# Optimization experiments

Measured on AMD Instinct MI355X. Metric: run time of the kernel, lower is better.

The kernel has to match this reference:

```python
import jax, jax.numpy as jnp
import numpy as np
from jax import lax

B, N, C_IN = 8, 4096, 64
NPOINT, NSAMPLE, RADIUS = 1024, 32, 0.2
BN_EPS = 1e-3  # keras BatchNormalization default epsilon


def _fps(pts):
    """Farthest point sampling on a single cloud pts: (N, 3) -> (NPOINT,) int32."""
    n = pts.shape[0]
    def step(carry, _):
        dist, far = carry
        c = pts[far]                                  # (3,)
        d = jnp.sum((pts - c) ** 2, axis=-1)          # (N,)
        dist = jnp.minimum(dist, d)
        nxt = jnp.argmax(dist).astype(jnp.int32)
        return (dist, nxt), far
    init = (jnp.full((n,), 1e10, pts.dtype), jnp.array(0, jnp.int32))
    _, idx = lax.scan(step, init, None, length=NPOINT)
    return idx


def _ball_query(xyz, new_xyz):
    """xyz: (B,N,3), new_xyz: (B,P,3) -> idx (B,P,NSAMPLE) int32.
    First NSAMPLE point indices within RADIUS of each centroid (in original
    order); slots beyond the in-ball count are filled with the first in-ball
    index, matching the PointNet++ CUDA query_ball_point semantics."""
    n = xyz.shape[1]
    # squared distances via the expansion trick to avoid a (B,P,N,3) temp
    d2 = (jnp.sum(new_xyz ** 2, -1)[:, :, None]
          + jnp.sum(xyz ** 2, -1)[:, None, :]
          - 2.0 * jnp.einsum('bpc,bnc->bpn', new_xyz, xyz))  # (B,P,N)
    in_ball = d2 < RADIUS ** 2
    cand = jnp.where(in_ball, jnp.arange(n, dtype=jnp.int32)[None, None, :], n)
    neg_top, _ = lax.top_k(-cand, NSAMPLE)   # NSAMPLE smallest indices
    idx = -neg_top                           # ascending order
    first = idx[..., :1]                     # centroid itself is always in-ball
    idx = jnp.where(idx == n, first, idx)
    return idx


def _group(feats, idx):
    """feats: (B,N,C), idx: (B,P,S) -> (B,P,S,C) gather per batch."""
    return jax.vmap(lambda f, i: f[i])(feats, idx)


def _mlp_layer(x, W, g, b, m, v):
    # 1x1 conv (no bias) + BN (inference stats) + ReLU
    x = jnp.einsum('bpsc,cd->bpsd', x, W)
    x = (x - m) * lax.rsqrt(v + BN_EPS) * g + b
    return jax.nn.relu(x)


def setup_inputs() -> dict:
    key = jax.random.key(0)
    ks = jax.random.split(key, 8)
    xyz = jax.random.uniform(ks[0], (B, N, 3), dtype=jnp.float32)
    points = jax.random.normal(ks[1], (B, N, C_IN), dtype=jnp.float32)
    c0 = 3 + C_IN  # use_xyz=True
    W0 = jax.random.normal(ks[2], (c0, 64), jnp.float32) / np.sqrt(c0)
    W1 = jax.random.normal(ks[3], (64, 64), jnp.float32) / np.sqrt(64.0)
    W2 = jax.random.normal(ks[4], (64, 128), jnp.float32) / np.sqrt(64.0)
    def bn(c):
        return (jnp.ones((c,), jnp.float32), jnp.zeros((c,), jnp.float32),
                jnp.zeros((c,), jnp.float32), jnp.ones((c,), jnp.float32))
    g0, b0, m0, v0 = bn(64)
    g1, b1, m1, v1 = bn(64)
    g2, b2, m2, v2 = bn(128)
    return dict(xyz=xyz, points=points,
                W0=W0, g0=g0, b0=b0, m0=m0, v0=v0,
                W1=W1, g1=g1, b1=b1, m1=m1, v1=v1,
                W2=W2, g2=g2, b2=b2, m2=m2, v2=v2)


def reference(xyz, points,
              W0, g0, b0, m0, v0,
              W1, g1, b1, m1, v1,
              W2, g2, b2, m2, v2):
    # --- sample_and_group ---
    fps_idx = jax.vmap(_fps)(xyz)                            # (B,P)
    new_xyz = jnp.take_along_axis(xyz, fps_idx[:, :, None], axis=1)  # (B,P,3)
    idx = _ball_query(xyz, new_xyz)                          # (B,P,S)
    grouped_xyz = _group(xyz, idx) - new_xyz[:, :, None, :]  # (B,P,S,3)
    grouped_pts = _group(points, idx)                        # (B,P,S,C)
    new_points = jnp.concatenate([grouped_xyz, grouped_pts], axis=-1)
    # --- shared per-point MLP (1x1 conv + BN + ReLU) ---
    new_points = _mlp_layer(new_points, W0, g0, b0, m0, v0)
    new_points = _mlp_layer(new_points, W1, g1, b1, m1, v1)
    new_points = _mlp_layer(new_points, W2, g2, b2, m2, v2)
    # --- max pool over the neighborhood axis ---
    new_points = jnp.max(new_points, axis=2)                 # (B,P,128)
    return new_xyz, new_points, idx
```

## Files before the change

### kernel.cpp

```cpp
#include <hip/hip_runtime.h>
#include <stdint.h>

#define BN_EPS 0.001f

typedef float v2f __attribute__((ext_vector_type(2)));


struct FpsSh {
  float px[4096], py[4096], pz[4096];
  unsigned long long wk[2][4];
  int curh[32];
};

struct WrkSh {
  float W0s[67 * 64];
  float W1s[64 * 64];
  float sh[64 * 36];
  float h0T[64 * 34];
  float s0c[64], t0c[64], s1c[64], t1c[64], s2c[128], t2c[128];
  float idxs[4 * 32];
  float cent[4 * 3];
};

union AllSh {
  FpsSh f;
  WrkSh w;
};

__global__ __launch_bounds__(256) void fused_kernel(
    const float* __restrict__ xyz, const float* __restrict__ points,
    const float* __restrict__ W0, const float* __restrict__ g0,
    const float* __restrict__ b0, const float* __restrict__ m0,
    const float* __restrict__ v0, const float* __restrict__ W1,
    const float* __restrict__ g1, const float* __restrict__ b1,
    const float* __restrict__ m1, const float* __restrict__ v1,
    const float* __restrict__ W2, const float* __restrict__ g2,
    const float* __restrict__ b2, const float* __restrict__ m2,
    const float* __restrict__ v2, float* __restrict__ new_xyz,
    float* __restrict__ new_points, float* __restrict__ idxf,
    unsigned int* __restrict__ prog) {
  __shared__ __align__(16) AllSh smem;
  const int bid = blockIdx.x;
  const int t = threadIdx.x;

  if (bid < 8) {
#pragma clang fp contract(off)
    float* px = smem.f.px;
    float* py = smem.f.py;
    float* pz = smem.f.pz;
    int* curh = smem.f.curh;
    auto& wk = smem.f.wk;
    const int lane = t & 63, wid = t >> 6;
    const int b = bid;
    const float* X = xyz + (size_t)b * 4096 * 3;
    float* out = new_xyz + (size_t)b * 1024 * 3;
    v2f x[8], y[8], z[8], dist[8];
#pragma unroll
    for (int j = 0; j < 8; ++j) {
      const int n0 = (2 * j) * 256 + t;
      const int n1 = (2 * j + 1) * 256 + t;
      x[j].x = X[n0 * 3 + 0]; x[j].y = X[n1 * 3 + 0];
      y[j].x = X[n0 * 3 + 1]; y[j].y = X[n1 * 3 + 1];
      z[j].x = X[n0 * 3 + 2]; z[j].y = X[n1 * 3 + 2];
      px[n0] = x[j].x; py[n0] = y[j].x; pz[n0] = z[j].x;
      px[n1] = x[j].y; py[n1] = y[j].y; pz[n1] = z[j].y;
      dist[j] = (v2f){1e10f, 1e10f};
    }
    __syncthreads();
    int cur = 0;
    for (int cc = 0; cc < 32; ++cc) {
      for (int ii = 0; ii < 32; ++ii) {
        const int it = cc * 32 + ii;
        if (t == 0) curh[ii] = cur;
        const float cx = px[cur], cy = py[cur], cz = pz[cur];
        const v2f cxv = {cx, cx}, cyv = {cy, cy}, czv = {cz, cz};
        float bestv = -1.0f;
        int bestj = 0;
#pragma unroll
        for (int j = 0; j < 8; ++j) {
          v2f dx = x[j] - cxv, dy = y[j] - cyv, dz = z[j] - czv;
          v2f d = dx * dx + dy * dy;
          d = d + dz * dz;
          v2f nd = __builtin_elementwise_min(dist[j], d);
          dist[j] = nd;
          if (nd.x > bestv) { bestv = nd.x; bestj = 2 * j; }
          if (nd.y > bestv) { bestv = nd.y; bestj = 2 * j + 1; }
        }
        const int besti = bestj * 256 + t;
        unsigned long long key =
            ((unsigned long long)__float_as_uint(bestv) << 32) | (unsigned)(~besti);
#define DPP_STEP(CTRL)                                                                     \
        {                                                                                  \
          unsigned lo_ = (unsigned)key, hi_ = (unsigned)(key >> 32);                       \
          unsigned ls = (unsigned)__builtin_amdgcn_update_dpp((int)lo_, (int)lo_, CTRL, 0xf, 0xf, false); \
          unsigned hs = (unsigned)__builtin_amdgcn_update_dpp((int)hi_, (int)hi_, CTRL, 0xf, 0xf, false); \
          unsigned long long sk = ((unsigned long long)hs << 32) | ls;                     \
          if (sk > key) key = sk;                                                          \
        }
        DPP_STEP(0x111)
        DPP_STEP(0x112)
        DPP_STEP(0x114)
        DPP_STEP(0x118)
        DPP_STEP(0x142)
        DPP_STEP(0x143)
#undef DPP_STEP
        const unsigned whi = (unsigned)__builtin_amdgcn_readlane((int)(key >> 32), 63);
        const unsigned wlo = (unsigned)__builtin_amdgcn_readlane((int)key, 63);
        if (lane == 0) wk[it & 1][wid] = ((unsigned long long)whi << 32) | wlo;
        __syncthreads();
        const unsigned long long k0 = wk[it & 1][0], k1 = wk[it & 1][1];
        const unsigned long long k2 = wk[it & 1][2], k3 = wk[it & 1][3];
        unsigned long long b01 = (k1 > k0) ? k1 : k0;
        unsigned long long b23 = (k3 > k2) ? k3 : k2;
        unsigned long long bk = (b23 > b01) ? b23 : b01;
        cur = (int)(~(unsigned)(bk & 0xffffffffull));
      }
      if (t < 32) {
        const int c = curh[t];
        const int p = cc * 32 + t;
        out[p * 3 + 0] = px[c];
        out[p * 3 + 1] = py[c];
        out[p * 3 + 2] = pz[c];
      }
      __syncthreads();
      if (t == 0)
        __hip_atomic_store(&prog[b * 32], (unsigned)(cc * 32 + 32),
                           __ATOMIC_RELEASE, __HIP_MEMORY_SCOPE_AGENT);
    }
    return;
  }

  float* W0s = smem.w.W0s;
  float* W1s = smem.w.W1s;
  float* s0c = smem.w.s0c; float* t0c = smem.w.t0c;
  float* s1c = smem.w.s1c; float* t1c = smem.w.t1c;
  float* s2c = smem.w.s2c; float* t2c = smem.w.t2c;
  for (int i = t; i < 67 * 64; i += 256) W0s[i] = W0[i];
  for (int i = t; i < 64 * 64; i += 256) W1s[i] = W1[i];
  if (t < 64) {
    float s = g0[t] * rsqrtf(v0[t] + BN_EPS); s0c[t] = s; t0c[t] = b0[t] - m0[t] * s;
    float u = g1[t] * rsqrtf(v1[t] + BN_EPS); s1c[t] = u; t1c[t] = b1[t] - m1[t] * u;
  }
  if (t < 128) {
    float s = g2[t] * rsqrtf(v2[t] + BN_EPS); s2c[t] = s; t2c[t] = b2[t] - m2[t] * s;
  }
  __syncthreads();
  const int sgrp = t & 15, dgrp = t >> 4;
  const int dg2 = t & 31, sg2 = t >> 5;
  float* inT = smem.w.sh;
  float* h1T = smem.w.sh;
  float* h0T = smem.w.h0T;
  float* pmax = h0T;

  int kbeg, kend, kstep;
  if (bid >= 256) { kbeg = 2032 + (bid - 256); kend = 2048; kstep = 8; }
  else            { kbeg = bid - 8;            kend = 2032; kstep = 248; }

  for (int k = kbeg; k < kend; k += kstep) {
    const int j = k >> 3, b = k & 7;
    const int pgbase = b * 1024 + j * 4;
    const unsigned need = (unsigned)(j * 4 + 4);
    {
      int guard = 0;
      while (__hip_atomic_load(&prog[b * 32], __ATOMIC_RELAXED,
                               __HIP_MEMORY_SCOPE_AGENT) < need) {
        __builtin_amdgcn_s_sleep(32);
        if (++guard > (1 << 20)) break;
      }
      (void)__hip_atomic_load(&prog[b * 32], __ATOMIC_ACQUIRE,
                              __HIP_MEMORY_SCOPE_AGENT);
    }
    {
#pragma clang fp contract(off)
      const int wv = t >> 6, lane = t & 63;
      const int pg = pgbase + wv;
      const float* X = xyz + (size_t)b * 4096 * 3;
      const float cx = new_xyz[pg * 3 + 0];
      const float cy = new_xyz[pg * 3 + 1];
      const float cz = new_xyz[pg * 3 + 2];
      const float csq = (cx * cx + cy * cy) + cz * cz;
      float* outg = idxf + (size_t)pg * 32;
      float* ol = smem.w.idxs + wv * 32;
      int total = 0;
      int first = -1;
      for (int chunk = 0; chunk < 64; ++chunk) {
        const int n = chunk * 64 + lane;
        const float xx = X[n * 3 + 0], yy = X[n * 3 + 1], zz = X[n * 3 + 2];
        const float sq = (xx * xx + yy * yy) + zz * zz;
        const float dot = fmaf(cz, zz, fmaf(cy, yy, cx * xx));
        const float d2 = (csq + sq) - 2.0f * dot;
        const bool in = d2 < 0.04f;
        const unsigned long long mask = __ballot(in);
        if (first < 0 && mask != 0ull) first = chunk * 64 + __builtin_ctzll(mask);
        if (in) {
          const int pos = total + __builtin_popcountll(mask & ((1ull << lane) - 1ull));
          if (pos < 32) { outg[pos] = (float)n; ol[pos] = (float)n; }
        }
        total += __builtin_popcountll(mask);
        if (total >= 32) break;
      }
      if (total < 32 && first >= 0) {
        const int slot = total + lane;
        if (slot < 32) { outg[slot] = (float)first; ol[slot] = (float)first; }
      }
      if (lane == 0) {
        smem.w.cent[wv * 3 + 0] = cx;
        smem.w.cent[wv * 3 + 1] = cy;
        smem.w.cent[wv * 3 + 2] = cz;
      }
    }
    __syncthreads();
    for (int pp = 0; pp < 4; ++pp) {
      const int pg = pgbase + pp;
      const float cx = smem.w.cent[pp * 3 + 0];
      const float cy = smem.w.cent[pp * 3 + 1];
      const float cz = smem.w.cent[pp * 3 + 2];
      {
        const int s = t >> 3, cg = t & 7;
        const int i = (int)smem.w.idxs[pp * 32 + s];
        const float* Pr = points + ((size_t)b * 4096 + i) * 64 + cg * 8;
        const float4 a = *(const float4*)Pr;
        const float4 c4 = *(const float4*)(Pr + 4);
        const int r = 3 + cg * 8;
        inT[(r + 0) * 34 + s] = a.x;  inT[(r + 1) * 34 + s] = a.y;
        inT[(r + 2) * 34 + s] = a.z;  inT[(r + 3) * 34 + s] = a.w;
        inT[(r + 4) * 34 + s] = c4.x; inT[(r + 5) * 34 + s] = c4.y;
        inT[(r + 6) * 34 + s] = c4.z; inT[(r + 7) * 34 + s] = c4.w;
        if (t < 32) {
          const int i2 = (int)smem.w.idxs[pp * 32 + t];
          const float* Xr = xyz + ((size_t)b * 4096 + i2) * 3;
          inT[0 * 34 + t] = Xr[0] - cx;
          inT[1 * 34 + t] = Xr[1] - cy;
          inT[2 * 34 + t] = Xr[2] - cz;
        }
      }
      __syncthreads();
      {
        float acc[2][4] = {{0, 0, 0, 0}, {0, 0, 0, 0}};
#pragma unroll 4
        for (int c = 0; c < 67; ++c) {
          const float2 a = *(const float2*)&inT[c * 34 + 2 * sgrp];
          const float4 w = *(const float4*)&W0s[c * 64 + 4 * dgrp];
          acc[0][0] = fmaf(a.x, w.x, acc[0][0]); acc[0][1] = fmaf(a.x, w.y, acc[0][1]);
          acc[0][2] = fmaf(a.x, w.z, acc[0][2]); acc[0][3] = fmaf(a.x, w.w, acc[0][3]);
          acc[1][0] = fmaf(a.y, w.x, acc[1][0]); acc[1][1] = fmaf(a.y, w.y, acc[1][1]);
          acc[1][2] = fmaf(a.y, w.z, acc[1][2]); acc[1][3] = fmaf(a.y, w.w, acc[1][3]);
        }
#pragma unroll
        for (int dj = 0; dj < 4; ++dj) {
          const int d = 4 * dgrp + dj;
          const float s = s0c[d], bb = t0c[d];
#pragma unroll
          for (int si = 0; si < 2; ++si) {
            float yv = fmaf(acc[si][dj], s, bb);
            h0T[d * 34 + 2 * sgrp + si] = fmaxf(yv, 0.0f);
          }
        }
      }
      __syncthreads();
      {
        float acc[2][4] = {{0, 0, 0, 0}, {0, 0, 0, 0}};
#pragma unroll 4
        for (int c = 0; c < 64; ++c) {
          const float2 a = *(const float2*)&h0T[c * 34 + 2 * sgrp];
          const float4 w = *(const float4*)&W1s[c * 64 + 4 * dgrp];
          acc[0][0] = fmaf(a.x, w.x, acc[0][0]); acc[0][1] = fmaf(a.x, w.y, acc[0][1]);
          acc[0][2] = fmaf(a.x, w.z, acc[0][2]); acc[0][3] = fmaf(a.x, w.w, acc[0][3]);
          acc[1][0] = fmaf(a.y, w.x, acc[1][0]); acc[1][1] = fmaf(a.y, w.y, acc[1][1]);
          acc[1][2] = fmaf(a.y, w.z, acc[1][2]); acc[1][3] = fmaf(a.y, w.w, acc[1][3]);
        }
#pragma unroll
        for (int dj = 0; dj < 4; ++dj) {
          const int d = 4 * dgrp + dj;
          const float s = s1c[d], bb = t1c[d];
#pragma unroll
          for (int si = 0; si < 2; ++si) {
            float yv = fmaf(acc[si][dj], s, bb);
            h1T[d * 36 + 2 * sgrp + si] = fmaxf(yv, 0.0f);
          }
        }
      }
      __syncthreads();
      {
        float acc[4][4] = {{0,0,0,0},{0,0,0,0},{0,0,0,0},{0,0,0,0}};
#pragma unroll 8
        for (int c = 0; c < 64; ++c) {
          const float4 a = *(const float4*)&h1T[c * 36 + 4 * sg2];
          const float4 w = *(const float4*)(W2 + c * 128 + 4 * dg2);
          acc[0][0] = fmaf(a.x, w.x, acc[0][0]); acc[0][1] = fmaf(a.x, w.y, acc[0][1]);
          acc[0][2] = fmaf(a.x, w.z, acc[0][2]); acc[0][3] = fmaf(a.x, w.w, acc[0][3]);
          acc[1][0] = fmaf(a.y, w.x, acc[1][0]); acc[1][1] = fmaf(a.y, w.y, acc[1][1]);
          acc[1][2] = fmaf(a.y, w.z, acc[1][2]); acc[1][3] = fmaf(a.y, w.w, acc[1][3]);
          acc[2][0] = fmaf(a.z, w.x, acc[2][0]); acc[2][1] = fmaf(a.z, w.y, acc[2][1]);
          acc[2][2] = fmaf(a.z, w.z, acc[2][2]); acc[2][3] = fmaf(a.z, w.w, acc[2][3]);
          acc[3][0] = fmaf(a.w, w.x, acc[3][0]); acc[3][1] = fmaf(a.w, w.y, acc[3][1]);
          acc[3][2] = fmaf(a.w, w.z, acc[3][2]); acc[3][3] = fmaf(a.w, w.w, acc[3][3]);
        }
#pragma unroll
        for (int dj = 0; dj < 4; ++dj) {
          const int d = 4 * dg2 + dj;
          const float s = s2c[d], bb = t2c[d];
          float mx = 0.0f;
#pragma unroll
          for (int si = 0; si < 4; ++si) {
            float yv = fmaf(acc[si][dj], s, bb);
            mx = fmaxf(mx, fmaxf(yv, 0.0f));
          }
          pmax[sg2 * 128 + d] = mx;
        }
      }
      __syncthreads();
      if (t < 128) {
        float mx = pmax[t];
#pragma unroll
        for (int g = 1; g < 8; ++g) mx = fmaxf(mx, pmax[g * 128 + t]);
        new_points[(size_t)pg * 128 + t] = mx;
      }
      __syncthreads();
    }
  }
}

extern "C" void kernel_launch(void* const* d_in, const int* in_sizes, int n_in,
                              void* d_out, int out_size, void* d_ws, size_t ws_size,
                              hipStream_t stream) {
  (void)in_sizes; (void)n_in; (void)out_size; (void)ws_size;
  const float* xyz    = (const float*)d_in[0];
  const float* points = (const float*)d_in[1];
  const float* W0 = (const float*)d_in[2];
  const float* g0 = (const float*)d_in[3];
  const float* b0 = (const float*)d_in[4];
  const float* m0 = (const float*)d_in[5];
  const float* v0 = (const float*)d_in[6];
  const float* W1 = (const float*)d_in[7];
  const float* g1 = (const float*)d_in[8];
  const float* b1 = (const float*)d_in[9];
  const float* m1 = (const float*)d_in[10];
  const float* v1 = (const float*)d_in[11];
  const float* W2 = (const float*)d_in[12];
  const float* g2 = (const float*)d_in[13];
  const float* b2 = (const float*)d_in[14];
  const float* m2 = (const float*)d_in[15];
  const float* v2 = (const float*)d_in[16];

  float* new_xyz    = (float*)d_out;
  float* new_points = new_xyz + 8 * 1024 * 3;
  float* idxf       = new_points + 8 * 1024 * 128;

  unsigned int* prog = (unsigned int*)d_ws;
  hipMemsetAsync(d_ws, 0, 8 * 32 * sizeof(unsigned int), stream);
  fused_kernel<<<264, 256, 0, stream>>>(xyz, points, W0, g0, b0, m0, v0,
                                        W1, g1, b1, m1, v1,
                                        W2, g2, b2, m2, v2,
                                        new_xyz, new_points, idxf, prog);
}
```

Measured before the change: 780.4 us.

## Split tail centroid groups across extra blocks and relax FPS progress signalling

The final 32 centroids per batch were previously handled as groups of four by 8 tail blocks, serialising the work after FPS finishes. The launch grows to 320 blocks so 64 tail blocks each handle one centroid, shortening the critical tail after the last FPS chunk. The progress flag publication changes from a release store to relaxed atomic stores plus an explicit s_waitcnt, and the consumer drops its acquire load in favour of relaxed atomic reads of new_xyz. The aim is to cut fence cost, but this relies on hardware ordering rather than the memory model, and the extra blocks need co-residency to avoid spin deadlock.

```diff
diff --git a/kernel.cpp b/kernel.cpp
--- a/kernel.cpp
+++ b/kernel.cpp
@@ -118,14 +118,19 @@
       if (t < 32) {
         const int c = curh[t];
         const int p = cc * 32 + t;
-        out[p * 3 + 0] = px[c];
-        out[p * 3 + 1] = py[c];
-        out[p * 3 + 2] = pz[c];
-      }
-      __syncthreads();
-      if (t == 0)
+        __hip_atomic_store(&out[p * 3 + 0], px[c], __ATOMIC_RELAXED,
+                           __HIP_MEMORY_SCOPE_AGENT);
+        __hip_atomic_store(&out[p * 3 + 1], py[c], __ATOMIC_RELAXED,
+                           __HIP_MEMORY_SCOPE_AGENT);
+        __hip_atomic_store(&out[p * 3 + 2], pz[c], __ATOMIC_RELAXED,
+                           __HIP_MEMORY_SCOPE_AGENT);
+      }
+      __syncthreads();
+      if (t == 0) {
+        asm volatile("s_waitcnt vmcnt(0)" ::: "memory");
         __hip_atomic_store(&prog[b * 32], (unsigned)(cc * 32 + 32),
-                           __ATOMIC_RELEASE, __HIP_MEMORY_SCOPE_AGENT);
+                           __ATOMIC_RELAXED, __HIP_MEMORY_SCOPE_AGENT);
+      }
     }
     return;
   }
@@ -152,66 +157,63 @@
   float* h0T = smem.w.h0T;
   float* pmax = h0T;
 
-  int kbeg, kend, kstep;
-  if (bid >= 256) { kbeg = 2032 + (bid - 256); kend = 2048; kstep = 8; }
-  else            { kbeg = bid - 8;            kend = 2032; kstep = 248; }
-
-  for (int k = kbeg; k < kend; k += kstep) {
-    const int j = k >> 3, b = k & 7;
-    const int pgbase = b * 1024 + j * 4;
-    const unsigned need = (unsigned)(j * 4 + 4);
-    {
-      int guard = 0;
-      while (__hip_atomic_load(&prog[b * 32], __ATOMIC_RELAXED,
-                               __HIP_MEMORY_SCOPE_AGENT) < need) {
-        __builtin_amdgcn_s_sleep(32);
-        if (++guard > (1 << 20)) break;
-      }
-      (void)__hip_atomic_load(&prog[b * 32], __ATOMIC_ACQUIRE,
-                              __HIP_MEMORY_SCOPE_AGENT);
-    }
+  auto wait_prog = [&](int b, unsigned need) {
+    int guard = 0;
+    while (__hip_atomic_load(&prog[b * 32], __ATOMIC_RELAXED,
+                             __HIP_MEMORY_SCOPE_AGENT) < need) {
+      __builtin_amdgcn_s_sleep(32);
+      if (++guard > (1 << 20)) break;
+    }
+  };
+
+  auto process_group = [&](int b, int p0, int nc) {
     {
 #pragma clang fp contract(off)
       const int wv = t >> 6, lane = t & 63;
-      const int pg = pgbase + wv;
-      const float* X = xyz + (size_t)b * 4096 * 3;
-      const float cx = new_xyz[pg * 3 + 0];
-      const float cy = new_xyz[pg * 3 + 1];
-      const float cz = new_xyz[pg * 3 + 2];
-      const float csq = (cx * cx + cy * cy) + cz * cz;
-      float* outg = idxf + (size_t)pg * 32;
-      float* ol = smem.w.idxs + wv * 32;
-      int total = 0;
-      int first = -1;
-      for (int chunk = 0; chunk < 64; ++chunk) {
-        const int n = chunk * 64 + lane;
-        const float xx = X[n * 3 + 0], yy = X[n * 3 + 1], zz = X[n * 3 + 2];
-        const float sq = (xx * xx + yy * yy) + zz * zz;
-        const float dot = fmaf(cz, zz, fmaf(cy, yy, cx * xx));
-        const float d2 = (csq + sq) - 2.0f * dot;
-        const bool in = d2 < 0.04f;
-        const unsigned long long mask = __ballot(in);
-        if (first < 0 && mask != 0ull) first = chunk * 64 + __builtin_ctzll(mask);
-        if (in) {
-          const int pos = total + __builtin_popcountll(mask & ((1ull << lane) - 1ull));
-          if (pos < 32) { outg[pos] = (float)n; ol[pos] = (float)n; }
-        }
-        total += __builtin_popcountll(mask);
-        if (total >= 32) break;
-      }
-      if (total < 32 && first >= 0) {
-        const int slot = total + lane;
-        if (slot < 32) { outg[slot] = (float)first; ol[slot] = (float)first; }
-      }
-      if (lane == 0) {
-        smem.w.cent[wv * 3 + 0] = cx;
-        smem.w.cent[wv * 3 + 1] = cy;
-        smem.w.cent[wv * 3 + 2] = cz;
+      if (wv < nc) {
+        const int pg = b * 1024 + p0 + wv;
+        const float* X = xyz + (size_t)b * 4096 * 3;
+        const float cx = __hip_atomic_load(&new_xyz[pg * 3 + 0], __ATOMIC_RELAXED,
+                                           __HIP_MEMORY_SCOPE_AGENT);
+        const float cy = __hip_atomic_load(&new_xyz[pg * 3 + 1], __ATOMIC_RELAXED,
+                                           __HIP_MEMORY_SCOPE_AGENT);
+        const float cz = __hip_atomic_load(&new_xyz[pg * 3 + 2], __ATOMIC_RELAXED,
+                                           __HIP_MEMORY_SCOPE_AGENT);
+        const float csq = (cx * cx + cy * cy) + cz * cz;
+        float* outg = idxf + (size_t)pg * 32;
+        float* ol = smem.w.idxs + wv * 32;
+        int total = 0;
+        int first = -1;
+        for (int chunk = 0; chunk < 64; ++chunk) {
+          const int n = chunk * 64 + lane;
+          const float xx = X[n * 3 + 0], yy = X[n * 3 + 1], zz = X[n * 3 + 2];
+          const float sq = (xx * xx + yy * yy) + zz * zz;
+          const float dot = fmaf(cz, zz, fmaf(cy, yy, cx * xx));
+          const float d2 = (csq + sq) - 2.0f * dot;
+          const bool in = d2 < 0.04f;
+          const unsigned long long mask = __ballot(in);
+          if (first < 0 && mask != 0ull) first = chunk * 64 + __builtin_ctzll(mask);
+          if (in) {
+            const int pos = total + __builtin_popcountll(mask & ((1ull << lane) - 1ull));
+            if (pos < 32) { outg[pos] = (float)n; ol[pos] = (float)n; }
+          }
+          total += __builtin_popcountll(mask);
+          if (total >= 32) break;
+        }
+        if (total < 32 && first >= 0) {
+          const int slot = total + lane;
+          if (slot < 32) { outg[slot] = (float)first; ol[slot] = (float)first; }
+        }
+        if (lane == 0) {
+          smem.w.cent[wv * 3 + 0] = cx;
+          smem.w.cent[wv * 3 + 1] = cy;
+          smem.w.cent[wv * 3 + 2] = cz;
+        }
       }
     }
     __syncthreads();
-    for (int pp = 0; pp < 4; ++pp) {
-      const int pg = pgbase + pp;
+    for (int pp = 0; pp < nc; ++pp) {
+      const int pg = b * 1024 + p0 + pp;
       const float cx = smem.w.cent[pp * 3 + 0];
       const float cy = smem.w.cent[pp * 3 + 1];
       const float cz = smem.w.cent[pp * 3 + 2];
@@ -317,6 +319,20 @@
         new_points[(size_t)pg * 128 + t] = mx;
       }
       __syncthreads();
+    }
+  };
+
+  if (bid >= 256) {
+    const int sid = bid - 256;
+    const int b = sid & 7;
+    const int p0 = 1016 + (sid >> 3);
+    wait_prog(b, (unsigned)(p0 + 1));
+    process_group(b, p0, 1);
+  } else {
+    for (int k = bid - 8; k < 2032; k += 248) {
+      const int j = k >> 3, b = k & 7;
+      wait_prog(b, (unsigned)(j * 4 + 4));
+      process_group(b, j * 4, 4);
     }
   }
 }
@@ -349,7 +365,7 @@
 
   unsigned int* prog = (unsigned int*)d_ws;
   hipMemsetAsync(d_ws, 0, 8 * 32 * sizeof(unsigned int), stream);
-  fused_kernel<<<264, 256, 0, stream>>>(xyz, points, W0, g0, b0, m0, v0,
+  fused_kernel<<<320, 256, 0, stream>>>(xyz, points, W0, g0, b0, m0, v0,
                                         W1, g1, b1, m1, v1,
                                         W2, g2, b2, m2, v2,
                                         new_xyz, new_points, idxf, prog);
```

Result: faster. 744.4 us (-4.6%).
